# Optimization experiments

Hardware: AMD Instinct MI355X
Metric: run time of the kernel (lower is better)

The kernel has to match this reference:

```python
import jax, jax.numpy as jnp
import numpy as np
import math

IN_C, OUT_C = 64, 128
OUT_C1 = int((OUT_C - IN_C) * 0.3 + IN_C)  # 83
OUT_C2 = int((OUT_C - IN_C) * 0.6 + IN_C)  # 102
OUT_C3 = OUT_C                              # 128
RESIDUE_RATIO = 0.5
R_RES = math.sqrt(RESIDUE_RATIO)
R_SC = math.sqrt(1.0 - RESIDUE_RATIO)
PRELU_INIT = 0.25
POST_MEAN = (1.0 - PRELU_INIT) / math.sqrt(2.0 * math.pi)
_POST_EX2 = (1.0 + PRELU_INIT ** 2) / 2.0
POST_STDV = math.sqrt(_POST_EX2 - POST_MEAN ** 2)


def _conv1x1_weight(key, out_c, in_c):
    # torch Conv1d custom init: normal_, then divide by per-out-channel L2 norm
    w = jax.random.normal(key, (out_c, in_c), dtype=jnp.float32)
    norm = jnp.sqrt(jnp.sum(w ** 2, axis=1, keepdims=True) + 1e-8)
    return w / norm


def cprelu(x, w):
    # x: [B, C, N], w: [C]
    y = jnp.where(x >= 0, x, x * w[None, :, None])
    return (y - POST_MEAN) / POST_STDV


def setup_inputs() -> dict:
    key = jax.random.key(0)
    ks = jax.random.split(key, 8)
    x = jax.random.normal(ks[0], (16, IN_C, 8192), dtype=jnp.float32)
    conn = jax.random.uniform(ks[1], (4096, 8192), dtype=jnp.float32)
    return {
        "x": x,
        "conn": conn,
        "w1": _conv1x1_weight(ks[2], OUT_C1, IN_C),
        "b1": jnp.zeros((OUT_C1,), jnp.float32),
        "p1": jnp.full((OUT_C1,), PRELU_INIT, jnp.float32),
        "w2": _conv1x1_weight(ks[3], OUT_C2, OUT_C1),
        "b2": jnp.zeros((OUT_C2,), jnp.float32),
        "p2": jnp.full((OUT_C2,), PRELU_INIT, jnp.float32),
        "wm": _conv1x1_weight(ks[4], OUT_C3, OUT_C2),
        "bm": jnp.zeros((OUT_C3,), jnp.float32),
        "p3": jnp.full((OUT_C3,), PRELU_INIT, jnp.float32),
        "ws": _conv1x1_weight(ks[5], OUT_C, IN_C),
        "bs": jnp.zeros((OUT_C,), jnp.float32),
    }


def _forward(x, conn, w1, b1, p1, w2, b2, p2, wm, bm, p3, ws, bs):
    # self-connection matrix: binary mask of per-row argmax entries (ties kept)
    sc = (conn - jnp.max(conn, axis=1, keepdims=True) >= 0).astype(jnp.float32)

    # residue branch: 1x1 conv -> CPReLU -> 1x1 conv -> CPReLU -> Meshconv -> CPReLU
    h = cprelu(jnp.einsum('bcn,oc->bon', x, w1) + b1[None, :, None], p1)
    h = cprelu(jnp.einsum('bcn,oc->bon', h, w2) + b2[None, :, None], p2)
    h = jnp.einsum('bcn,oc->bon', h, wm) + bm[None, :, None]      # [B, C3, Nin]
    h = jnp.einsum('oi,bci->bco', conn, h)                         # mesh pooling -> [B, C3, Nout]
    res = cprelu(h, p3)

    # shortcut branch: Meshconv with self_connection_matrix (1x1 conv + pooled gather)
    s = jnp.einsum('bcn,oc->bon', x, ws) + bs[None, :, None]       # [B, OUT_C, Nin]
    s = jnp.einsum('oi,bci->bco', sc, s)                           # [B, OUT_C, Nout]

    return s * R_SC + res * R_RES


def reference(x, conn, w1, b1, p1, w2, b2, p2, wm, bm, p3, ws, bs):
    return _forward(x, conn, w1, b1, p1, w2, b2, p2, wm, bm, p3, ws, bs)
```

## Files before the change

kernel.cpp:

```cpp
#include <hip/hip_runtime.h>
#include <hip/hip_bf16.h>
#include <stdint.h>

using bf16x8 = __attribute__((ext_vector_type(8))) __bf16;
using bf16x4 = __attribute__((ext_vector_type(4))) __bf16;
using f32x4  = __attribute__((ext_vector_type(4))) float;

typedef const uint32_t __attribute__((address_space(1)))* gas_ptr;
typedef uint32_t __attribute__((address_space(3)))* las_ptr;

__device__ __forceinline__ void load_lds16(const void* g, void* l) {
    __builtin_amdgcn_global_load_lds((gas_ptr)g, (las_ptr)l, 16, 0, 0);
}

#define PM  0.29920671030107454f
#define PIS 1.5046096f
#define RHALF 0.70710678118654752f

__global__ __launch_bounds__(256) void k_prep(const float* __restrict__ w1,
                                              const float* __restrict__ w2,
                                              const float* __restrict__ wm,
                                              const float* __restrict__ wsw,
                                              __bf16* __restrict__ W1p,
                                              __bf16* __restrict__ W2p,
                                              __bf16* __restrict__ WMp,
                                              __bf16* __restrict__ WSp)
{
    const int id = blockIdx.x * 256 + threadIdx.x;
    const int stride = gridDim.x * 256;
    for (int i = id; i < 96 * 64; i += stride) {
        int oc = i >> 6, ic = i & 63;
        W1p[i] = (__bf16)((oc < 83) ? w1[oc * 64 + ic] : 0.f);
    }
    for (int i = id; i < 112 * 96; i += stride) {
        int oc = i / 96, ic = i % 96;
        W2p[i] = (__bf16)((oc < 102 && ic < 83) ? w2[oc * 83 + ic] : 0.f);
    }
    for (int i = id; i < 128 * 128; i += stride) {
        int oc = i >> 7, ic = i & 127;
        WMp[i] = (__bf16)((ic < 102) ? wm[oc * 102 + ic] : 0.f);
    }
    for (int i = id; i < 128 * 64; i += stride) {
        WSp[i] = (__bf16)wsw[i];
    }
}

__global__ __launch_bounds__(256) void k_conv(const float* __restrict__ conn,
                                              __bf16* __restrict__ cb,
                                              size_t rowstride,
                                              int* __restrict__ cnt,
                                              int* __restrict__ idx)
{
    const int o = blockIdx.x;
    const int t = threadIdx.x;
    const float* row = conn + (size_t)o * 8192;
    float4 v[8];
    float m = -1e30f;
#pragma unroll
    for (int q = 0; q < 8; q++) {
        v[q] = *(const float4*)(row + (size_t)(q * 256 + t) * 4);
        m = fmaxf(m, fmaxf(fmaxf(v[q].x, v[q].y), fmaxf(v[q].z, v[q].w)));
    }
    __syncthreads();
    __bf16* drow = cb + (size_t)o * rowstride;
#pragma unroll
    for (int q = 0; q < 8; q++) {
        bf16x4 w;
        w[0] = (__bf16)v[q].x; w[1] = (__bf16)v[q].y;
        w[2] = (__bf16)v[q].z; w[3] = (__bf16)v[q].w;
        *(bf16x4*)(drow + (size_t)(q * 256 + t) * 4) = w;
    }
#pragma unroll
    for (int off = 32; off > 0; off >>= 1) m = fmaxf(m, __shfl_down(m, off, 64));
    __shared__ float wmax[4];
    __shared__ int scnt;
    if ((t & 63) == 0) wmax[t >> 6] = m;
    if (t == 0) scnt = 0;
    __syncthreads();
    const float rmax = fmaxf(fmaxf(wmax[0], wmax[1]), fmaxf(wmax[2], wmax[3]));
#pragma unroll
    for (int q = 0; q < 8; q++) {
        float vv[4] = {v[q].x, v[q].y, v[q].z, v[q].w};
#pragma unroll
        for (int e = 0; e < 4; e++) {
            if (vv[e] >= rmax) {
                int p = atomicAdd(&scnt, 1);
                if (p < 16) idx[o * 16 + p] = (q * 256 + t) * 4 + e;
            }
        }
    }
    __syncthreads();
    if (t == 0) cnt[o] = scnt < 16 ? scnt : 16;
}

template<int KS>
__device__ __forceinline__ f32x4 mfma_tile(const __bf16* __restrict__ W, int wstride, int mt,
                                           const __bf16* B, int bstride, int nt, int lane)
{
    f32x4 acc = {0.f, 0.f, 0.f, 0.f};
    const int l15 = lane & 15;
    const int kg  = (lane >> 4) << 3;
    const __bf16* wp = W + (mt * 16 + l15) * wstride + kg;
    const __bf16* bp = B + (nt * 16 + l15) * bstride + kg;
#pragma unroll
    for (int ks = 0; ks < KS; ks++) {
        bf16x8 av = *(const bf16x8*)(wp + ks * 32);
        bf16x8 bv = *(const bf16x8*)(bp + ks * 32);
        acc = __builtin_amdgcn_mfma_f32_16x16x32_bf16(av, bv, acc, 0, 0, 0);
    }
    return acc;
}

__global__ __launch_bounds__(256) void k_chain(
    const float* __restrict__ x,
    const float* __restrict__ b1, const float* __restrict__ p1,
    const float* __restrict__ b2, const float* __restrict__ p2,
    const float* __restrict__ bm, const float* __restrict__ bs,
    const __bf16* __restrict__ W1p, const __bf16* __restrict__ W2p,
    const __bf16* __restrict__ WMp, const __bf16* __restrict__ WSp,
    __bf16* __restrict__ h3, __bf16* __restrict__ s_t)
{
    __shared__ __bf16 buf0[128 * 136];
    __shared__ __bf16 H1t[128 * 104];
    __shared__ float  bl[672];
    float* b1l = bl;       float* p1l = bl + 96;
    float* b2l = bl + 192; float* p2l = bl + 304;
    float* bml = bl + 416; float* bsl = bl + 544;

    const int t = threadIdx.x, lane = t & 63, wid = t >> 6;
    const int b = blockIdx.y;
    const int p0 = blockIdx.x * 128;

    for (int i = t; i < 96; i += 256)  { b1l[i] = (i < 83)  ? b1[i] : 0.f; p1l[i] = (i < 83)  ? p1[i] : 0.f; }
    for (int i = t; i < 112; i += 256) { b2l[i] = (i < 102) ? b2[i] : 0.f; p2l[i] = (i < 102) ? p2[i] : 0.f; }
    for (int i = t; i < 128; i += 256) { bml[i] = bm[i]; bsl[i] = bs[i]; }

    {
        const int p = t & 127;
        const int chalf = t >> 7;
#pragma unroll 4
        for (int it = 0; it < 32; it++) {
            int c = it * 2 + chalf;
            buf0[p * 72 + c] = (__bf16)x[((size_t)b * 64 + c) * 8192 + p0 + p];
        }
    }
    __syncthreads();

    const int quad4 = (lane >> 4) << 2;
    const int l15 = lane & 15;

    for (int tt = wid; tt < 64; tt += 4) {
        int mt = tt >> 3, nt = tt & 7;
        f32x4 a = mfma_tile<2>(WSp, 64, mt, buf0, 72, nt, lane);
        int ocb = mt * 16 + quad4;
        int pos = nt * 16 + l15;
        bf16x4 ov;
#pragma unroll
        for (int r = 0; r < 4; r++) ov[r] = (__bf16)(a[r] + bsl[ocb + r]);
        *(bf16x4*)(s_t + ((size_t)b * 8192 + p0 + pos) * 128 + ocb) = ov;
    }
    for (int tt = wid; tt < 48; tt += 4) {
        int mt = tt / 8, nt = tt % 8;
        f32x4 a = mfma_tile<2>(W1p, 64, mt, buf0, 72, nt, lane);
        int ocb = mt * 16 + quad4;
        int pos = nt * 16 + l15;
        bf16x4 ov;
#pragma unroll
        for (int r = 0; r < 4; r++) {
            float v = a[r] + b1l[ocb + r];
            v = (v >= 0.f) ? v : v * p1l[ocb + r];
            ov[r] = (__bf16)((v - PM) * PIS);
        }
        *(bf16x4*)(&H1t[pos * 104 + ocb]) = ov;
    }
    __syncthreads();

    for (int tt = wid; tt < 56; tt += 4) {
        int mt = tt / 8, nt = tt % 8;
        f32x4 a = mfma_tile<3>(W2p, 96, mt, H1t, 104, nt, lane);
        int ocb = mt * 16 + quad4;
        int pos = nt * 16 + l15;
        bf16x4 ov;
#pragma unroll
        for (int r = 0; r < 4; r++) {
            float v = a[r] + b2l[ocb + r];
            v = (v >= 0.f) ? v : v * p2l[ocb + r];
            ov[r] = (__bf16)((v - PM) * PIS);
        }
        *(bf16x4*)(&buf0[pos * 136 + ocb]) = ov;
    }
    for (int i = t; i < 128 * 16; i += 256) {
        int pos = i >> 4, c = 112 + (i & 15);
        buf0[pos * 136 + c] = (__bf16)0.f;
    }
    __syncthreads();

    for (int tt = wid; tt < 64; tt += 4) {
        int mt = tt >> 3, nt = tt & 7;
        f32x4 a = mfma_tile<4>(WMp, 128, mt, buf0, 136, nt, lane);
        int ocb = mt * 16 + quad4;
        int pos = nt * 16 + l15;
#pragma unroll
        for (int r = 0; r < 4; r++)
            h3[((size_t)b * 128 + ocb + r) * 8192 + p0 + pos] = (__bf16)(a[r] + bml[ocb + r]);
    }
}

__global__ __launch_bounds__(256) void k_gemm(const __bf16* __restrict__ A,
                                              const __bf16* __restrict__ B,
                                              size_t bstride,
                                              float* __restrict__ C)
{
    __shared__ __bf16 la[128 * 32];
    __shared__ __bf16 lb[128 * 32];
    const int t = threadIdx.x;
    const int lane = t & 63;
    const int wid = t >> 6;
    const int tM = blockIdx.y * 128;
    const int tN = blockIdx.x * 128;
    const int wm2 = (wid & 1) * 64;
    const int wn2 = (wid >> 1) * 64;

    f32x4 acc[4][4];
    const f32x4 zero = {0.f, 0.f, 0.f, 0.f};
#pragma unroll
    for (int i = 0; i < 4; i++)
#pragma unroll
        for (int j = 0; j < 4; j++) acc[i][j] = zero;

    const __bf16* Ab = A + (size_t)tM * 8192;
    const __bf16* Bb = B + (size_t)tN * bstride;
    const int ar = t >> 2;
    const int ak = ((t & 3) ^ ((t >> 3) & 3)) * 8;
    const int l15 = lane & 15;
    const int q = lane >> 4;

    int aoff[4], boff[4];
#pragma unroll
    for (int i = 0; i < 4; i++) {
        int row = wm2 + i * 16 + l15;
        aoff[i] = row * 32 + ((q ^ ((row >> 1) & 3)) * 8);
    }
#pragma unroll
    for (int j = 0; j < 4; j++) {
        int row = wn2 + j * 16 + l15;
        boff[j] = row * 32 + ((q ^ ((row >> 1) & 3)) * 8);
    }

    for (int kt = 0; kt < 8192; kt += 32) {
        load_lds16(Ab + (size_t)ar * 8192 + kt + ak, la + t * 8);
        load_lds16(Ab + (size_t)(64 + ar) * 8192 + kt + ak, la + 2048 + t * 8);
        load_lds16(Bb + (size_t)ar * bstride + kt + ak, lb + t * 8);
        load_lds16(Bb + (size_t)(64 + ar) * bstride + kt + ak, lb + 2048 + t * 8);
        __syncthreads();
        bf16x8 af[4], bfr[4];
#pragma unroll
        for (int i = 0; i < 4; i++) af[i]  = *(const bf16x8*)(la + aoff[i]);
#pragma unroll
        for (int j = 0; j < 4; j++) bfr[j] = *(const bf16x8*)(lb + boff[j]);
#pragma unroll
        for (int i = 0; i < 4; i++)
#pragma unroll
            for (int j = 0; j < 4; j++)
                acc[i][j] = __builtin_amdgcn_mfma_f32_16x16x32_bf16(af[i], bfr[j], acc[i][j], 0, 0, 0);
        __syncthreads();
    }

    const int quad4 = (lane >> 4) * 4;
#pragma unroll
    for (int i = 0; i < 4; i++) {
        int gm = tM + wm2 + i * 16 + quad4;
#pragma unroll
        for (int j = 0; j < 4; j++) {
            int gn = tN + wn2 + j * 16 + l15;
#pragma unroll
            for (int r = 0; r < 4; r++)
                C[(size_t)(gm + r) * 4096 + gn] = acc[i][j][r];
        }
    }
}

__global__ __launch_bounds__(256) void k_combine(float* __restrict__ out,
                                                 const __bf16* __restrict__ s_t,
                                                 const int* __restrict__ idx,
                                                 const int* __restrict__ cnt,
                                                 const float* __restrict__ p3)
{
    __shared__ float sp[64][133];
    const int b = blockIdx.y;
    const int o0 = blockIdx.x * 64;
    const int t = threadIdx.x;

    {
        const int ol = t >> 2;
        const int part = t & 3;
        const int o = o0 + ol;
        const int n = cnt[o];
        float acc[32];
#pragma unroll
        for (int j = 0; j < 32; j++) acc[j] = 0.f;
        for (int k = 0; k < n; k++) {
            const int i = idx[o * 16 + k];
            const __bf16* row = s_t + ((size_t)b * 8192 + i) * 128 + part * 32;
#pragma unroll
            for (int j = 0; j < 32; j += 8) {
                bf16x8 v = *(const bf16x8*)(row + j);
#pragma unroll
                for (int u = 0; u < 8; u++) acc[j + u] += (float)v[u];
            }
        }
#pragma unroll
        for (int j = 0; j < 32; j++) sp[ol][part * 32 + j] = acc[j];
    }
    __syncthreads();

    for (int rr = 0; rr < 32; rr++) {
        const int c = rr * 4 + (t >> 6);
        const int o = t & 63;
        const size_t oi = ((size_t)b * 128 + c) * 4096 + o0 + o;
        float v = out[oi];
        const float pw = p3[c];
        float y = (v >= 0.f) ? v : v * pw;
        y = (y - PM) * PIS;
        out[oi] = sp[o][c] * RHALF + y * RHALF;
    }
}

extern "C" void kernel_launch(void* const* d_in, const int* in_sizes, int n_in,
                              void* d_out, int out_size, void* d_ws, size_t ws_size,
                              hipStream_t stream) {
    (void)in_sizes; (void)n_in; (void)out_size;
    const float* x    = (const float*)d_in[0];
    const float* conn = (const float*)d_in[1];
    const float* w1   = (const float*)d_in[2];
    const float* b1   = (const float*)d_in[3];
    const float* p1   = (const float*)d_in[4];
    const float* w2   = (const float*)d_in[5];
    const float* b2   = (const float*)d_in[6];
    const float* p2   = (const float*)d_in[7];
    const float* wm   = (const float*)d_in[8];
    const float* bm   = (const float*)d_in[9];
    const float* p3   = (const float*)d_in[10];
    const float* wsw  = (const float*)d_in[11];
    const float* bs   = (const float*)d_in[12];
    float* out = (float*)d_out;

    char* ws = (char*)d_ws;
    __bf16* h3  = (__bf16*)(ws);
    __bf16* s_t = (__bf16*)(ws + 33554432);
    __bf16* W1p = (__bf16*)(ws + 67108864);
    __bf16* W2p = (__bf16*)(ws + 67108864 + 12288);
    __bf16* WMp = (__bf16*)(ws + 67108864 + 33792);
    __bf16* WSp = (__bf16*)(ws + 67108864 + 66560);
    int* idx = (int*)(ws + 67108864 + 82944);
    int* cnt = (int*)(ws + 67108864 + 82944 + 262144);

    const size_t connb_off = 67108864 + 82944 + 262144 + 16384;
    __bf16* connb;
    size_t  cstride;
    if (ws_size >= connb_off + (size_t)4096 * 8192 * 2) {
        connb = (__bf16*)(ws + connb_off);
        cstride = 8192;
    } else {
        connb = (__bf16*)const_cast<float*>(conn);
        cstride = 16384;
    }

    k_prep<<<32, 256, 0, stream>>>(w1, w2, wm, wsw, W1p, W2p, WMp, WSp);
    k_conv<<<4096, 256, 0, stream>>>(conn, connb, cstride, cnt, idx);
    k_chain<<<dim3(8192 / 128, 16), 256, 0, stream>>>(x, b1, p1, b2, p2, bm, bs,
                                                      W1p, W2p, WMp, WSp, h3, s_t);
    k_gemm<<<dim3(4096 / 128, 2048 / 128), 256, 0, stream>>>(h3, connb, cstride, out);
    k_combine<<<dim3(4096 / 64, 16), 256, 0, stream>>>(out, s_t, idx, cnt, p3);
}
```

Measured before the change: 549.3 us.

## Split-K the pooling GEMM into two halves and halve chain tile width

The large mesh-pooling GEMM (M=2048, N=4096, K=8192) is split along K into two grid slices. Each slice writes a separate fp32 partial, and the combine kernel sums the two partials before applying PReLU. The goal is to double the block count (512 to 1024) for better occupancy across the CUs, at the cost of an extra 32MB partial buffer write and read. Separately, the chain kernel tile drops from 128 to 64 positions, which gives more blocks and less LDS per block.

Result: faster. 523.4 us (-4.7%).

```diff
diff --git a/kernel.cpp b/kernel.cpp
--- a/kernel.cpp
+++ b/kernel.cpp
@@ -120,8 +120,8 @@
     const __bf16* __restrict__ WMp, const __bf16* __restrict__ WSp,
     __bf16* __restrict__ h3, __bf16* __restrict__ s_t)
 {
-    __shared__ __bf16 buf0[128 * 136];
-    __shared__ __bf16 H1t[128 * 104];
+    __shared__ __bf16 buf0[64 * 136];
+    __shared__ __bf16 H1t[64 * 104];
     __shared__ float  bl[672];
     float* b1l = bl;       float* p1l = bl + 96;
     float* b2l = bl + 192; float* p2l = bl + 304;
@@ -129,18 +129,18 @@
 
     const int t = threadIdx.x, lane = t & 63, wid = t >> 6;
     const int b = blockIdx.y;
-    const int p0 = blockIdx.x * 128;
+    const int p0 = blockIdx.x * 64;
 
     for (int i = t; i < 96; i += 256)  { b1l[i] = (i < 83)  ? b1[i] : 0.f; p1l[i] = (i < 83)  ? p1[i] : 0.f; }
     for (int i = t; i < 112; i += 256) { b2l[i] = (i < 102) ? b2[i] : 0.f; p2l[i] = (i < 102) ? p2[i] : 0.f; }
     for (int i = t; i < 128; i += 256) { bml[i] = bm[i]; bsl[i] = bs[i]; }
 
     {
-        const int p = t & 127;
-        const int chalf = t >> 7;
+        const int p = t & 63;
+        const int cg = t >> 6;
 #pragma unroll 4
-        for (int it = 0; it < 32; it++) {
-            int c = it * 2 + chalf;
+        for (int it = 0; it < 16; it++) {
+            int c = it * 4 + cg;
             buf0[p * 72 + c] = (__bf16)x[((size_t)b * 64 + c) * 8192 + p0 + p];
         }
     }
@@ -149,8 +149,8 @@
     const int quad4 = (lane >> 4) << 2;
     const int l15 = lane & 15;
 
-    for (int tt = wid; tt < 64; tt += 4) {
-        int mt = tt >> 3, nt = tt & 7;
+    for (int tt = wid; tt < 32; tt += 4) {
+        int mt = tt >> 2, nt = tt & 3;
         f32x4 a = mfma_tile<2>(WSp, 64, mt, buf0, 72, nt, lane);
         int ocb = mt * 16 + quad4;
         int pos = nt * 16 + l15;
@@ -159,8 +159,8 @@
         for (int r = 0; r < 4; r++) ov[r] = (__bf16)(a[r] + bsl[ocb + r]);
         *(bf16x4*)(s_t + ((size_t)b * 8192 + p0 + pos) * 128 + ocb) = ov;
     }
-    for (int tt = wid; tt < 48; tt += 4) {
-        int mt = tt / 8, nt = tt % 8;
+    for (int tt = wid; tt < 24; tt += 4) {
+        int mt = tt >> 2, nt = tt & 3;
         f32x4 a = mfma_tile<2>(W1p, 64, mt, buf0, 72, nt, lane);
         int ocb = mt * 16 + quad4;
         int pos = nt * 16 + l15;
@@ -175,8 +175,8 @@
     }
     __syncthreads();
 
-    for (int tt = wid; tt < 56; tt += 4) {
-        int mt = tt / 8, nt = tt % 8;
+    for (int tt = wid; tt < 28; tt += 4) {
+        int mt = tt >> 2, nt = tt & 3;
         f32x4 a = mfma_tile<3>(W2p, 96, mt, H1t, 104, nt, lane);
         int ocb = mt * 16 + quad4;
         int pos = nt * 16 + l15;
@@ -189,14 +189,14 @@
         }
         *(bf16x4*)(&buf0[pos * 136 + ocb]) = ov;
     }
-    for (int i = t; i < 128 * 16; i += 256) {
+    for (int i = t; i < 64 * 16; i += 256) {
         int pos = i >> 4, c = 112 + (i & 15);
         buf0[pos * 136 + c] = (__bf16)0.f;
     }
     __syncthreads();
 
-    for (int tt = wid; tt < 64; tt += 4) {
-        int mt = tt >> 3, nt = tt & 7;
+    for (int tt = wid; tt < 32; tt += 4) {
+        int mt = tt >> 2, nt = tt & 3;
         f32x4 a = mfma_tile<4>(WMp, 128, mt, buf0, 136, nt, lane);
         int ocb = mt * 16 + quad4;
         int pos = nt * 16 + l15;
@@ -209,7 +209,9 @@
 __global__ __launch_bounds__(256) void k_gemm(const __bf16* __restrict__ A,
                                               const __bf16* __restrict__ B,
                                               size_t bstride,
-                                              float* __restrict__ C)
+                                              float* __restrict__ C0,
+                                              float* __restrict__ C1,
+                                              int KH)
 {
     __shared__ __bf16 la[128 * 32];
     __shared__ __bf16 lb[128 * 32];
@@ -218,6 +220,9 @@
     const int wid = t >> 6;
     const int tM = blockIdx.y * 128;
     const int tN = blockIdx.x * 128;
+    const int kz = blockIdx.z;
+    const int k0 = kz * KH;
+    float* __restrict__ C = kz ? C1 : C0;
     const int wm2 = (wid & 1) * 64;
     const int wn2 = (wid >> 1) * 64;
 
@@ -247,7 +252,7 @@
         boff[j] = row * 32 + ((q ^ ((row >> 1) & 3)) * 8);
     }
 
-    for (int kt = 0; kt < 8192; kt += 32) {
+    for (int kt = k0; kt < k0 + KH; kt += 32) {
         load_lds16(Ab + (size_t)ar * 8192 + kt + ak, la + t * 8);
         load_lds16(Ab + (size_t)(64 + ar) * 8192 + kt + ak, la + 2048 + t * 8);
         load_lds16(Bb + (size_t)ar * bstride + kt + ak, lb + t * 8);
@@ -281,6 +286,8 @@
 }
 
 __global__ __launch_bounds__(256) void k_combine(float* __restrict__ out,
+                                                 const float* __restrict__ P1,
+                                                 int nsplit,
                                                  const __bf16* __restrict__ s_t,
                                                  const int* __restrict__ idx,
                                                  const int* __restrict__ cnt,
@@ -314,15 +321,28 @@
     }
     __syncthreads();
 
-    for (int rr = 0; rr < 32; rr++) {
-        const int c = rr * 4 + (t >> 6);
-        const int o = t & 63;
-        const size_t oi = ((size_t)b * 128 + c) * 4096 + o0 + o;
-        float v = out[oi];
-        const float pw = p3[c];
-        float y = (v >= 0.f) ? v : v * pw;
-        y = (y - PM) * PIS;
-        out[oi] = sp[o][c] * RHALF + y * RHALF;
+    if (nsplit == 2) {
+        for (int rr = 0; rr < 32; rr++) {
+            const int c = rr * 4 + (t >> 6);
+            const int o = t & 63;
+            const size_t oi = ((size_t)b * 128 + c) * 4096 + o0 + o;
+            float v = out[oi] + P1[oi];
+            const float pw = p3[c];
+            float y = (v >= 0.f) ? v : v * pw;
+            y = (y - PM) * PIS;
+            out[oi] = sp[o][c] * RHALF + y * RHALF;
+        }
+    } else {
+        for (int rr = 0; rr < 32; rr++) {
+            const int c = rr * 4 + (t >> 6);
+            const int o = t & 63;
+            const size_t oi = ((size_t)b * 128 + c) * 4096 + o0 + o;
+            float v = out[oi];
+            const float pw = p3[c];
+            float y = (v >= 0.f) ? v : v * pw;
+            y = (y - PM) * PIS;
+            out[oi] = sp[o][c] * RHALF + y * RHALF;
+        }
     }
 }
 
@@ -354,8 +374,10 @@
     __bf16* WSp = (__bf16*)(ws + 67108864 + 66560);
     int* idx = (int*)(ws + 67108864 + 82944);
     int* cnt = (int*)(ws + 67108864 + 82944 + 262144);
-
-    const size_t connb_off = 67108864 + 82944 + 262144 + 16384;
+    const size_t p1_off    = 67108864 + 82944 + 262144 + 16384;
+    float* Pk1 = (float*)(ws + p1_off);
+    const size_t connb_off = p1_off + 33554432;
+
     __bf16* connb;
     size_t  cstride;
     if (ws_size >= connb_off + (size_t)4096 * 8192 * 2) {
@@ -365,11 +387,14 @@
         connb = (__bf16*)const_cast<float*>(conn);
         cstride = 16384;
     }
+    const int nsplit = (ws_size >= p1_off + 33554432) ? 2 : 1;
+    const int KH = 8192 / nsplit;
 
     k_prep<<<32, 256, 0, stream>>>(w1, w2, wm, wsw, W1p, W2p, WMp, WSp);
     k_conv<<<4096, 256, 0, stream>>>(conn, connb, cstride, cnt, idx);
-    k_chain<<<dim3(8192 / 128, 16), 256, 0, stream>>>(x, b1, p1, b2, p2, bm, bs,
-                                                      W1p, W2p, WMp, WSp, h3, s_t);
-    k_gemm<<<dim3(4096 / 128, 2048 / 128), 256, 0, stream>>>(h3, connb, cstride, out);
-    k_combine<<<dim3(4096 / 64, 16), 256, 0, stream>>>(out, s_t, idx, cnt, p3);
-}
+    k_chain<<<dim3(8192 / 64, 16), 256, 0, stream>>>(x, b1, p1, b2, p2, bm, bs,
+                                                     W1p, W2p, WMp, WSp, h3, s_t);
+    k_gemm<<<dim3(4096 / 128, 2048 / 128, nsplit), 256, 0, stream>>>(h3, connb, cstride,
+                                                                     out, Pk1, KH);
+    k_combine<<<dim3(4096 / 64, 16), 256, 0, stream>>>(out, Pk1, nsplit, s_t, idx, cnt, p3);
+}
```
